# Performance work log

Hardware: AMD Instinct MI355X
Metric: run time of the kernel (lower is better)

## Reference

```python
import jax, jax.numpy as jnp
import numpy as np

B, L = 4096, 200
N_USERS, N_ITEMS, N_CATS, N_DUR = 200000, 500000, 1000, 20
D = 64  # item_embed_dim == seq_embed_dim


def _lin(k, din, dout):
    kw, kb = jax.random.split(k)
    s = 1.0 / np.sqrt(din)
    return (jax.random.uniform(kw, (din, dout), minval=-s, maxval=s),
            jax.random.uniform(kb, (dout,), minval=-s, maxval=s))


def setup_inputs() -> dict:
    key = jax.random.key(0)
    ks = jax.random.split(key, 20)
    inp = {
        'user_id': jax.random.randint(ks[0], (B,), 0, N_USERS),
        'item_id': jax.random.randint(ks[1], (B,), 0, N_ITEMS),
        'item_category': jax.random.randint(ks[2], (B,), 0, N_CATS),
        'item_dur_bkt': jax.random.randint(ks[3], (B,), 0, N_DUR),
        'user_dense': jax.random.normal(ks[4], (B, 25), dtype=jnp.float32),
        'item_dense': jax.random.normal(ks[5], (B, 3), dtype=jnp.float32),
        'history_seq': jax.random.randint(ks[6], (B, L), 0, N_ITEMS + 1),
        # embedding tables (init std=0.01 as in _init_weights)
        'user_W': 0.01 * jax.random.normal(ks[7], (N_USERS, 64), dtype=jnp.float32),
        'item_W': 0.01 * jax.random.normal(ks[8], (N_ITEMS, D), dtype=jnp.float32),
        'cat_W': 0.01 * jax.random.normal(ks[9], (N_CATS, 16), dtype=jnp.float32),
        'dur_W': 0.01 * jax.random.normal(ks[10], (N_DUR, 8), dtype=jnp.float32),
        'hist_W': 0.01 * jax.random.normal(ks[11], (N_ITEMS + 1, D), dtype=jnp.float32),
    }
    # attention MLP: 4*D=256 -> 64 -> 32 -> 1
    inp['aW0'], inp['ab0'] = _lin(ks[12], 4 * D, 64)
    inp['aW1'], inp['ab1'] = _lin(ks[13], 64, 32)
    inp['aW2'], inp['ab2'] = _lin(ks[14], 32, 1)
    # final MLP: concat_dim 64+64+16+8+25+3+64 = 244 -> 256 -> 128 -> 1
    inp['mW0'], inp['mb0'] = _lin(ks[15], 244, 256)
    inp['mW1'], inp['mb1'] = _lin(ks[16], 256, 128)
    inp['mW2'], inp['mb2'] = _lin(ks[17], 128, 1)
    return inp


def reference(user_id, item_id, item_category, item_dur_bkt, user_dense, item_dense,
              history_seq, user_W, item_W, cat_W, dur_W, hist_W,
              aW0, ab0, aW1, ab1, aW2, ab2, mW0, mb0, mW1, mb1, mW2, mb2):
    u_emb = user_W[user_id]            # (B, 64)
    i_emb = item_W[item_id]            # (B, D)
    c_emb = cat_W[item_category]       # (B, 16)
    d_emb = dur_W[item_dur_bkt]        # (B, 8)
    hist = hist_W[history_seq]         # (B, L, D)

    t = i_emb[:, None, :]              # (B, 1, D); item_dim == seq_dim so no slice
    tb = jnp.broadcast_to(t, hist.shape)
    feat = jnp.concatenate([hist, tb, hist * t, hist - t], axis=-1)  # (B, L, 4D)

    h = jax.nn.relu(feat @ aW0 + ab0)
    h = jax.nn.relu(h @ aW1 + ab1)
    scores = (h @ aW2 + ab2)[..., 0]   # (B, L)

    pad_mask = history_seq == 0
    scores = jnp.where(pad_mask, jnp.float32(-1e9), scores)
    w = jax.nn.softmax(scores, axis=-1)                # (B, L)
    pooled = jnp.einsum('bl,bld->bd', w, hist)         # (B, D)

    x = jnp.concatenate([u_emb, i_emb, c_emb, d_emb, user_dense, item_dense, pooled], axis=-1)
    h = jax.nn.relu(x @ mW0 + mb0)     # dropout is identity in eval mode
    h = jax.nn.relu(h @ mW1 + mb1)
    logit = (h @ mW2 + mb2)[..., 0]
    return jax.nn.sigmoid(logit)       # (B,)
```

## Files before the change

kernel.cpp:

```cpp
#include <hip/hip_runtime.h>
#include <hip/hip_bf16.h>

#define L_SZ 200
#define RB 8
#define HS_STRIDE 72

typedef __attribute__((ext_vector_type(8))) short short8;
typedef __attribute__((ext_vector_type(4))) float floatx4;

__device__ __forceinline__ unsigned short f2bf(float f) {
    unsigned int u = __float_as_uint(f);
    unsigned int r = (u + 0x7fffu + ((u >> 16) & 1u)) >> 16;
    return (unsigned short)r;
}
__device__ __forceinline__ float bf2f(unsigned short h) {
    return __uint_as_float(((unsigned int)h) << 16);
}
__device__ __forceinline__ float wave_sum64(float v) {
    #pragma unroll
    for (int m = 1; m <= 32; m <<= 1) v += __shfl_xor(v, m, 64);
    return v;
}
__device__ __forceinline__ float wave_max64(float v) {
    #pragma unroll
    for (int m = 1; m <= 32; m <<= 1) v = fmaxf(v, __shfl_xor(v, m, 64));
    return v;
}
__device__ __forceinline__ unsigned int pk2(float a, float b) {
    return ((unsigned int)f2bf(b) << 16) | (unsigned int)f2bf(a);
}

__global__ __launch_bounds__(256, 4) void attn_kernel(
    const int* __restrict__ item_id, const int* __restrict__ hist_seq,
    const float* __restrict__ item_W, const float* __restrict__ hist_W,
    const float* __restrict__ aW0, const float* __restrict__ ab0,
    const float* __restrict__ aW1, const float* __restrict__ ab1,
    const float* __restrict__ aW2, const float* __restrict__ ab2,
    float* __restrict__ pooled_ws)
{
    __shared__ __align__(16) unsigned char smem[39136];
    unsigned short* Hs  = (unsigned short*)(smem);
    unsigned short* BB  = (unsigned short*)(smem + 28800);
    int*   seq_sh = (int*)(smem + 36992);
    float* scores = (float*)(smem + 37792);
    float* iemb   = (float*)(smem + 38592);
    float* cb     = (float*)(smem + 38848);
    float* red    = (float*)(smem + 39104);

    const int tid  = threadIdx.x;
    const int w    = tid >> 6;
    const int lane = tid & 63;
    const int b    = blockIdx.x;
    const int* hseq = hist_seq + b * L_SZ;

    if (tid < 64)   iemb[tid]   = item_W[(size_t)item_id[b] * 64 + tid];
    if (tid < L_SZ) seq_sh[tid] = hseq[tid];
    __syncthreads();

    for (int u = tid; u < L_SZ * 8; u += 256) {
        int row = u >> 3, c8 = u & 7;
        const float* src = hist_W + (size_t)seq_sh[row] * 64 + c8 * 8;
        float4 f0 = *(const float4*)src;
        float4 f1 = *(const float4*)(src + 4);
        uint4 pk;
        pk.x = pk2(f0.x, f0.y); pk.y = pk2(f0.z, f0.w);
        pk.z = pk2(f1.x, f1.y); pk.w = pk2(f1.z, f1.w);
        *(uint4*)(Hs + row * HS_STRIDE + c8 * 8) = pk;
    }
    for (int u = tid; u < 512; u += 256) {
        int j = u >> 3, k8 = u & 7;
        float v[8];
        #pragma unroll
        for (int i = 0; i < 8; ++i) {
            int k = k8 * 8 + i;
            v[i] = aW0[k * 64 + j] + aW0[(192 + k) * 64 + j]
                 + iemb[k] * aW0[(128 + k) * 64 + j];
        }
        uint4 pk;
        pk.x = pk2(v[0], v[1]); pk.y = pk2(v[2], v[3]);
        pk.z = pk2(v[4], v[5]); pk.w = pk2(v[6], v[7]);
        *(uint4*)(BB + j * 64 + (k8 ^ (j & 7)) * 8) = pk;
    }
    if (w < 2) {
        float cpart = 0.f;
        #pragma unroll 4
        for (int t = 0; t < 32; ++t) {
            int k = w * 32 + t;
            cpart = fmaf(iemb[k], aW0[(64 + k) * 64 + lane] - aW0[(192 + k) * 64 + lane], cpart);
        }
        scores[w * 64 + lane] = cpart;
    }
    const int c = lane & 15, q = lane >> 4;
    short8 bW1[2][2];
    #pragma unroll
    for (int nt = 0; nt < 2; ++nt)
        #pragma unroll
        for (int ks = 0; ks < 2; ++ks) {
            unsigned short tmp[8];
            #pragma unroll
            for (int i = 0; i < 8; ++i)
                tmp[i] = f2bf(aW1[(ks * 32 + q * 8 + i) * 32 + nt * 16 + c]);
            bW1[nt][ks] = *(short8*)tmp;
        }
    float ab1r[2], aw2r[2];
    #pragma unroll
    for (int nt = 0; nt < 2; ++nt) {
        ab1r[nt] = ab1[nt * 16 + c];
        aw2r[nt] = aW2[nt * 16 + c];
    }
    const float ab2s = ab2[0];
    __syncthreads();

    short8 bW[4][2];
    #pragma unroll
    for (int nt = 0; nt < 4; ++nt)
        #pragma unroll
        for (int ks = 0; ks < 2; ++ks)
            bW[nt][ks] = *(const short8*)(BB + (nt * 16 + c) * 64
                                             + ((4 * ks + q) ^ (c & 7)) * 8);
    if (tid < 64)
        cb[tid] = ab0[tid] + scores[tid] + scores[64 + tid];
    __syncthreads();

    float cbr[4];
    #pragma unroll
    for (int nt = 0; nt < 4; ++nt) cbr[nt] = cb[nt * 16 + c];
    unsigned short* scrw = BB + w * (16 * 64);
    const floatx4 zf = {0.f, 0.f, 0.f, 0.f};

    for (int mt = w; mt < 13; mt += 4) {
        const int rowbase = mt * 16;
        floatx4 acc0[4] = {zf, zf, zf, zf};
        #pragma unroll
        for (int ks = 0; ks < 2; ++ks) {
            short8 a = *(const short8*)(Hs + (rowbase + c) * HS_STRIDE + ks * 32 + q * 8);
            acc0[0] = __builtin_amdgcn_mfma_f32_16x16x32_bf16(a, bW[0][ks], acc0[0], 0, 0, 0);
            acc0[1] = __builtin_amdgcn_mfma_f32_16x16x32_bf16(a, bW[1][ks], acc0[1], 0, 0, 0);
            acc0[2] = __builtin_amdgcn_mfma_f32_16x16x32_bf16(a, bW[2][ks], acc0[2], 0, 0, 0);
            acc0[3] = __builtin_amdgcn_mfma_f32_16x16x32_bf16(a, bW[3][ks], acc0[3], 0, 0, 0);
        }
        #pragma unroll
        for (int nt = 0; nt < 4; ++nt)
            #pragma unroll
            for (int r = 0; r < 4; ++r) {
                float h = fmaxf(acc0[nt][r] + cbr[nt], 0.f);
                int row = q * 4 + r;
                int gp = (2 * nt + (c >> 3)) ^ (row & 7);
                scrw[row * 64 + gp * 8 + (c & 7)] = f2bf(h);
            }
        floatx4 acc1[2] = {zf, zf};
        #pragma unroll
        for (int ks = 0; ks < 2; ++ks) {
            short8 a1 = *(const short8*)(scrw + c * 64 + ((4 * ks + q) ^ (c & 7)) * 8);
            acc1[0] = __builtin_amdgcn_mfma_f32_16x16x32_bf16(a1, bW1[0][ks], acc1[0], 0, 0, 0);
            acc1[1] = __builtin_amdgcn_mfma_f32_16x16x32_bf16(a1, bW1[1][ks], acc1[1], 0, 0, 0);
        }
        float s[4];
        #pragma unroll
        for (int r = 0; r < 4; ++r)
            s[r] = fmaxf(acc1[0][r] + ab1r[0], 0.f) * aw2r[0]
                 + fmaxf(acc1[1][r] + ab1r[1], 0.f) * aw2r[1];
        #pragma unroll
        for (int m = 1; m <= 8; m <<= 1)
            #pragma unroll
            for (int r = 0; r < 4; ++r) s[r] += __shfl_xor(s[r], m, 64);
        if (c == 0) {
            #pragma unroll
            for (int r = 0; r < 4; ++r) {
                int l = rowbase + q * 4 + r;
                if (l < L_SZ)
                    scores[l] = (seq_sh[l] == 0) ? -1.0e9f : (s[r] + ab2s);
            }
        }
    }
    __syncthreads();

    float s0 = (tid < L_SZ) ? scores[tid] : -3.0e38f;
    float mx = wave_max64(s0);
    if (lane == 0) red[w] = mx;
    __syncthreads();
    mx = fmaxf(fmaxf(red[0], red[1]), fmaxf(red[2], red[3]));
    float e = (tid < L_SZ) ? __expf(s0 - mx) : 0.f;
    float sm = wave_sum64(e);
    if (lane == 0) red[4 + w] = sm;
    __syncthreads();
    const float winv = 1.f / ((red[4] + red[5]) + (red[6] + red[7]));
    if (tid < L_SZ) scores[tid] = e * winv;
    __syncthreads();

    float* pools = (float*)BB;
    {
        int g  = (w << 1) | (lane >> 5);
        int jj = lane & 31;
        int l0 = g * 26, l1 = (l0 + 26 < L_SZ) ? l0 + 26 : L_SZ;
        float p0 = 0.f, p1 = 0.f;
        for (int l = l0; l < l1; ++l) {
            float wt = scores[l];
            unsigned int pv = *(const unsigned int*)(Hs + l * HS_STRIDE + jj * 2);
            p0 = fmaf(wt, bf2f((unsigned short)(pv & 0xffffu)), p0);
            p1 = fmaf(wt, bf2f((unsigned short)(pv >> 16)), p1);
        }
        float2 pp = {p0, p1};
        *(float2*)&pools[g * 64 + jj * 2] = pp;
    }
    __syncthreads();
    if (tid < 64) {
        float sum = 0.f;
        #pragma unroll
        for (int g = 0; g < 8; ++g) sum += pools[g * 64 + tid];
        pooled_ws[(size_t)b * 64 + tid] = sum;
    }
}

__global__ __launch_bounds__(256) void mlp_kernel(
    const int* __restrict__ user_id, const int* __restrict__ item_id,
    const int* __restrict__ item_cat, const int* __restrict__ item_dur,
    const float* __restrict__ user_dense, const float* __restrict__ item_dense,
    const float* __restrict__ user_W, const float* __restrict__ item_W,
    const float* __restrict__ cat_W, const float* __restrict__ dur_W,
    const float* __restrict__ mW0, const float* __restrict__ mb0,
    const float* __restrict__ mW1, const float* __restrict__ mb1,
    const float* __restrict__ mW2, const float* __restrict__ mb2,
    const float* __restrict__ pooled_ws, float* __restrict__ out)
{
    __shared__ __align__(16) float xT[244][RB];
    __shared__ __align__(16) float h0T[256][RB];
    __shared__ __align__(16) float h1T[128][RB];
    __shared__ __align__(16) float part[128][RB];

    const int tid = threadIdx.x;
    const int b0 = blockIdx.x * RB;

    for (int idx = tid; idx < 244 * RB; idx += 256) {
        int r = idx / 244;
        int c = idx - r * 244;
        int b = b0 + r;
        float v;
        if (c < 64)       v = user_W[(size_t)user_id[b] * 64 + c];
        else if (c < 128) v = item_W[(size_t)item_id[b] * 64 + (c - 64)];
        else if (c < 144) v = cat_W[item_cat[b] * 16 + (c - 128)];
        else if (c < 152) v = dur_W[item_dur[b] * 8 + (c - 144)];
        else if (c < 177) v = user_dense[b * 25 + (c - 152)];
        else if (c < 180) v = item_dense[b * 3 + (c - 177)];
        else              v = pooled_ws[(size_t)b * 64 + (c - 180)];
        xT[c][r] = v;
    }
    __syncthreads();

    {
        float acc[RB];
        const float bias = mb0[tid];
        #pragma unroll
        for (int r = 0; r < RB; ++r) acc[r] = bias;
        #pragma unroll 4
        for (int k = 0; k < 244; ++k) {
            float wk = mW0[k * 256 + tid];
            float4 xa = *(const float4*)&xT[k][0];
            float4 xb = *(const float4*)&xT[k][4];
            acc[0] = fmaf(wk, xa.x, acc[0]);
            acc[1] = fmaf(wk, xa.y, acc[1]);
            acc[2] = fmaf(wk, xa.z, acc[2]);
            acc[3] = fmaf(wk, xa.w, acc[3]);
            acc[4] = fmaf(wk, xb.x, acc[4]);
            acc[5] = fmaf(wk, xb.y, acc[5]);
            acc[6] = fmaf(wk, xb.z, acc[6]);
            acc[7] = fmaf(wk, xb.w, acc[7]);
        }
        #pragma unroll
        for (int r = 0; r < RB; ++r) h0T[tid][r] = fmaxf(acc[r], 0.f);
    }
    __syncthreads();

    const int jj = tid & 127;
    const int half = tid >> 7;
    {
        float acc[RB];
        #pragma unroll
        for (int r = 0; r < RB; ++r) acc[r] = 0.f;
        #pragma unroll 4
        for (int t = 0; t < 128; ++t) {
            int k = half * 128 + t;
            float wk = mW1[k * 128 + jj];
            float4 ha = *(const float4*)&h0T[k][0];
            float4 hb = *(const float4*)&h0T[k][4];
            acc[0] = fmaf(wk, ha.x, acc[0]);
            acc[1] = fmaf(wk, ha.y, acc[1]);
            acc[2] = fmaf(wk, ha.z, acc[2]);
            acc[3] = fmaf(wk, ha.w, acc[3]);
            acc[4] = fmaf(wk, hb.x, acc[4]);
            acc[5] = fmaf(wk, hb.y, acc[5]);
            acc[6] = fmaf(wk, hb.z, acc[6]);
            acc[7] = fmaf(wk, hb.w, acc[7]);
        }
        if (half == 1) {
            #pragma unroll
            for (int r = 0; r < RB; ++r) part[jj][r] = acc[r];
        }
        __syncthreads();
        if (half == 0) {
            const float bias = mb1[jj];
            #pragma unroll
            for (int r = 0; r < RB; ++r)
                h1T[jj][r] = fmaxf(acc[r] + part[jj][r] + bias, 0.f);
        }
    }
    __syncthreads();

    if (tid < RB) {
        const int r = tid;
        float a0 = mb2[0], a1 = 0.f;
        #pragma unroll 8
        for (int k = 0; k < 128; k += 2) {
            a0 = fmaf(h1T[k][r],     mW2[k],     a0);
            a1 = fmaf(h1T[k + 1][r], mW2[k + 1], a1);
        }
        float a = a0 + a1;
        out[b0 + r] = 1.f / (1.f + __expf(-a));
    }
}

extern "C" void kernel_launch(void* const* d_in, const int* in_sizes, int n_in,
                              void* d_out, int out_size, void* d_ws, size_t ws_size,
                              hipStream_t stream) {
    (void)in_sizes; (void)n_in; (void)out_size; (void)ws_size;
    const int*   user_id    = (const int*)d_in[0];
    const int*   item_id    = (const int*)d_in[1];
    const int*   item_cat   = (const int*)d_in[2];
    const int*   item_dur   = (const int*)d_in[3];
    const float* user_dense = (const float*)d_in[4];
    const float* item_dense = (const float*)d_in[5];
    const int*   hist_seq   = (const int*)d_in[6];
    const float* user_W     = (const float*)d_in[7];
    const float* item_W     = (const float*)d_in[8];
    const float* cat_W      = (const float*)d_in[9];
    const float* dur_W      = (const float*)d_in[10];
    const float* hist_W     = (const float*)d_in[11];
    const float* aW0 = (const float*)d_in[12];
    const float* ab0 = (const float*)d_in[13];
    const float* aW1 = (const float*)d_in[14];
    const float* ab1 = (const float*)d_in[15];
    const float* aW2 = (const float*)d_in[16];
    const float* ab2 = (const float*)d_in[17];
    const float* mW0 = (const float*)d_in[18];
    const float* mb0 = (const float*)d_in[19];
    const float* mW1 = (const float*)d_in[20];
    const float* mb1 = (const float*)d_in[21];
    const float* mW2 = (const float*)d_in[22];
    const float* mb2 = (const float*)d_in[23];
    float* out = (float*)d_out;
    float* pooled_ws = (float*)d_ws;

    attn_kernel<<<4096, 256, 0, stream>>>(item_id, hist_seq, item_W, hist_W,
                                          aW0, ab0, aW1, ab1, aW2, ab2, pooled_ws);
    mlp_kernel<<<4096 / RB, 256, 0, stream>>>(user_id, item_id, item_cat, item_dur,
                                              user_dense, item_dense,
                                              user_W, item_W, cat_W, dur_W,
                                              mW0, mb0, mW1, mb1, mW2, mb2,
                                              pooled_ws, out);
}
```

Before: 431.2 us.

## Gather history rows directly into MFMA A-fragments and drop sync stages

Each wave now gathers its own history rows from global memory straight into registers shaped as MFMA A operands. It packs them to bf16 and uses them directly for the first attention layer, storing a swizzled copy to shared memory only for the pooling step. The shared item-embedding and sequence buffers, one barrier and the serial gather-then-convert phase are removed, and the hist loads are issued early to overlap with the weight preparation. The cost is higher register pressure from holding up to four tiles of gathered floats per thread, which may reduce occupancy.

```diff
diff --git a/kernel.cpp b/kernel.cpp
--- a/kernel.cpp
+++ b/kernel.cpp
@@ -3,7 +3,6 @@
 
 #define L_SZ 200
 #define RB 8
-#define HS_STRIDE 72
 
 typedef __attribute__((ext_vector_type(8))) short short8;
 typedef __attribute__((ext_vector_type(4))) float floatx4;
@@ -38,43 +37,71 @@
     const float* __restrict__ aW2, const float* __restrict__ ab2,
     float* __restrict__ pooled_ws)
 {
-    __shared__ __align__(16) unsigned char smem[39136];
-    unsigned short* Hs  = (unsigned short*)(smem);
-    unsigned short* BB  = (unsigned short*)(smem + 28800);
-    int*   seq_sh = (int*)(smem + 36992);
-    float* scores = (float*)(smem + 37792);
-    float* iemb   = (float*)(smem + 38592);
-    float* cb     = (float*)(smem + 38848);
-    float* red    = (float*)(smem + 39104);
+    __shared__ __align__(16) unsigned char smem[35136];
+    unsigned short* Hs = (unsigned short*)(smem);
+    unsigned short* BB = (unsigned short*)(smem + 25600);
+    float* scores = (float*)(smem + 33792);
+    float* cbp    = (float*)(smem + 34592);
+    float* red    = (float*)(smem + 35104);
 
     const int tid  = threadIdx.x;
     const int w    = tid >> 6;
     const int lane = tid & 63;
+    const int c    = lane & 15, q = lane >> 4;
     const int b    = blockIdx.x;
-    const int* hseq = hist_seq + b * L_SZ;
-
-    if (tid < 64)   iemb[tid]   = item_W[(size_t)item_id[b] * 64 + tid];
-    if (tid < L_SZ) seq_sh[tid] = hseq[tid];
-    __syncthreads();
-
-    for (int u = tid; u < L_SZ * 8; u += 256) {
-        int row = u >> 3, c8 = u & 7;
-        const float* src = hist_W + (size_t)seq_sh[row] * 64 + c8 * 8;
-        float4 f0 = *(const float4*)src;
-        float4 f1 = *(const float4*)(src + 4);
-        uint4 pk;
-        pk.x = pk2(f0.x, f0.y); pk.y = pk2(f0.z, f0.w);
-        pk.z = pk2(f1.x, f1.y); pk.w = pk2(f1.z, f1.w);
-        *(uint4*)(Hs + row * HS_STRIDE + c8 * 8) = pk;
-    }
+    const int item = item_id[b];
+    const float* iW = item_W + (size_t)item * 64;
+
+    const int ntile = (w == 0) ? 4 : 3;
+
+    int    seqr[4];
+    float4 g0[4][2], g1[4][2];
+    #pragma unroll
+    for (int t = 0; t < 4; ++t) {
+        if (t < ntile) {
+            const int mt  = w + 4 * t;
+            const int row = mt * 16 + c;
+            const int rc  = (row < L_SZ) ? row : (L_SZ - 1);
+            seqr[t] = hist_seq[b * L_SZ + rc];
+            const float* hrow = hist_W + (size_t)seqr[t] * 64;
+            #pragma unroll
+            for (int ks = 0; ks < 2; ++ks) {
+                g0[t][ks] = *(const float4*)(hrow + ks * 32 + q * 8);
+                g1[t][ks] = *(const float4*)(hrow + ks * 32 + q * 8 + 4);
+            }
+        }
+    }
+
+    short8 bW1[2][2];
+    #pragma unroll
+    for (int nt = 0; nt < 2; ++nt)
+        #pragma unroll
+        for (int ks = 0; ks < 2; ++ks) {
+            unsigned short tmp[8];
+            #pragma unroll
+            for (int i = 0; i < 8; ++i)
+                tmp[i] = f2bf(aW1[(ks * 32 + q * 8 + i) * 32 + nt * 16 + c]);
+            bW1[nt][ks] = *(short8*)tmp;
+        }
+    float ab1r[2], aw2r[2];
+    #pragma unroll
+    for (int nt = 0; nt < 2; ++nt) {
+        ab1r[nt] = ab1[nt * 16 + c];
+        aw2r[nt] = aW2[nt * 16 + c];
+    }
+    const float ab2s = ab2[0];
+
     for (int u = tid; u < 512; u += 256) {
         int j = u >> 3, k8 = u & 7;
+        float4 ia = *(const float4*)(iW + k8 * 8);
+        float4 ib = *(const float4*)(iW + k8 * 8 + 4);
+        float ie[8] = {ia.x, ia.y, ia.z, ia.w, ib.x, ib.y, ib.z, ib.w};
         float v[8];
         #pragma unroll
         for (int i = 0; i < 8; ++i) {
             int k = k8 * 8 + i;
             v[i] = aW0[k * 64 + j] + aW0[(192 + k) * 64 + j]
-                 + iemb[k] * aW0[(128 + k) * 64 + j];
+                 + ie[i] * aW0[(128 + k) * 64 + j];
         }
         uint4 pk;
         pk.x = pk2(v[0], v[1]); pk.y = pk2(v[2], v[3]);
@@ -86,29 +113,30 @@
         #pragma unroll 4
         for (int t = 0; t < 32; ++t) {
             int k = w * 32 + t;
-            cpart = fmaf(iemb[k], aW0[(64 + k) * 64 + lane] - aW0[(192 + k) * 64 + lane], cpart);
-        }
-        scores[w * 64 + lane] = cpart;
-    }
-    const int c = lane & 15, q = lane >> 4;
-    short8 bW1[2][2];
-    #pragma unroll
-    for (int nt = 0; nt < 2; ++nt)
-        #pragma unroll
-        for (int ks = 0; ks < 2; ++ks) {
-            unsigned short tmp[8];
-            #pragma unroll
-            for (int i = 0; i < 8; ++i)
-                tmp[i] = f2bf(aW1[(ks * 32 + q * 8 + i) * 32 + nt * 16 + c]);
-            bW1[nt][ks] = *(short8*)tmp;
-        }
-    float ab1r[2], aw2r[2];
-    #pragma unroll
-    for (int nt = 0; nt < 2; ++nt) {
-        ab1r[nt] = ab1[nt * 16 + c];
-        aw2r[nt] = aW2[nt * 16 + c];
-    }
-    const float ab2s = ab2[0];
+            cpart = fmaf(iW[k], aW0[(64 + k) * 64 + lane] - aW0[(192 + k) * 64 + lane], cpart);
+        }
+        cbp[w * 64 + lane] = cpart;
+    }
+
+    short8 afr[4][2];
+    #pragma unroll
+    for (int t = 0; t < 4; ++t) {
+        if (t < ntile) {
+            const int mt  = w + 4 * t;
+            const int row = mt * 16 + c;
+            #pragma unroll
+            for (int ks = 0; ks < 2; ++ks) {
+                uint4 pk;
+                pk.x = pk2(g0[t][ks].x, g0[t][ks].y);
+                pk.y = pk2(g0[t][ks].z, g0[t][ks].w);
+                pk.z = pk2(g1[t][ks].x, g1[t][ks].y);
+                pk.w = pk2(g1[t][ks].z, g1[t][ks].w);
+                afr[t][ks] = *(short8*)&pk;
+                if (row < L_SZ)
+                    *(uint4*)(Hs + row * 64 + ((ks * 4 + q) ^ (row & 7)) * 8) = pk;
+            }
+        }
+    }
     __syncthreads();
 
     short8 bW[4][2];
@@ -118,26 +146,29 @@
         for (int ks = 0; ks < 2; ++ks)
             bW[nt][ks] = *(const short8*)(BB + (nt * 16 + c) * 64
                                              + ((4 * ks + q) ^ (c & 7)) * 8);
-    if (tid < 64)
-        cb[tid] = ab0[tid] + scores[tid] + scores[64 + tid];
-    __syncthreads();
-
     float cbr[4];
     #pragma unroll
-    for (int nt = 0; nt < 4; ++nt) cbr[nt] = cb[nt * 16 + c];
+    for (int nt = 0; nt < 4; ++nt) {
+        int j = nt * 16 + c;
+        cbr[nt] = ab0[j] + cbp[j] + cbp[64 + j];
+    }
+    __syncthreads();
+
     unsigned short* scrw = BB + w * (16 * 64);
     const floatx4 zf = {0.f, 0.f, 0.f, 0.f};
 
-    for (int mt = w; mt < 13; mt += 4) {
+    #pragma unroll
+    for (int t = 0; t < 4; ++t) {
+        if (t >= ntile) break;
+        const int mt = w + 4 * t;
         const int rowbase = mt * 16;
         floatx4 acc0[4] = {zf, zf, zf, zf};
         #pragma unroll
         for (int ks = 0; ks < 2; ++ks) {
-            short8 a = *(const short8*)(Hs + (rowbase + c) * HS_STRIDE + ks * 32 + q * 8);
-            acc0[0] = __builtin_amdgcn_mfma_f32_16x16x32_bf16(a, bW[0][ks], acc0[0], 0, 0, 0);
-            acc0[1] = __builtin_amdgcn_mfma_f32_16x16x32_bf16(a, bW[1][ks], acc0[1], 0, 0, 0);
-            acc0[2] = __builtin_amdgcn_mfma_f32_16x16x32_bf16(a, bW[2][ks], acc0[2], 0, 0, 0);
-            acc0[3] = __builtin_amdgcn_mfma_f32_16x16x32_bf16(a, bW[3][ks], acc0[3], 0, 0, 0);
+            acc0[0] = __builtin_amdgcn_mfma_f32_16x16x32_bf16(afr[t][ks], bW[0][ks], acc0[0], 0, 0, 0);
+            acc0[1] = __builtin_amdgcn_mfma_f32_16x16x32_bf16(afr[t][ks], bW[1][ks], acc0[1], 0, 0, 0);
+            acc0[2] = __builtin_amdgcn_mfma_f32_16x16x32_bf16(afr[t][ks], bW[2][ks], acc0[2], 0, 0, 0);
+            acc0[3] = __builtin_amdgcn_mfma_f32_16x16x32_bf16(afr[t][ks], bW[3][ks], acc0[3], 0, 0, 0);
         }
         #pragma unroll
         for (int nt = 0; nt < 4; ++nt)
@@ -164,13 +195,13 @@
         for (int m = 1; m <= 8; m <<= 1)
             #pragma unroll
             for (int r = 0; r < 4; ++r) s[r] += __shfl_xor(s[r], m, 64);
-        if (c == 0) {
-            #pragma unroll
-            for (int r = 0; r < 4; ++r) {
-                int l = rowbase + q * 4 + r;
-                if (l < L_SZ)
-                    scores[l] = (seq_sh[l] == 0) ? -1.0e9f : (s[r] + ab2s);
-            }
+        int rsel = c & 3;
+        float sv = (rsel == 0) ? s[0] : (rsel == 1) ? s[1] : (rsel == 2) ? s[2] : s[3];
+        sv = __shfl(sv, ((c >> 2) << 4) | c, 64);
+        if (q == 0) {
+            int l = rowbase + c;
+            if (l < L_SZ)
+                scores[l] = (seqr[t] == 0) ? -1.0e9f : (sv + ab2s);
         }
     }
     __syncthreads();
@@ -196,7 +227,8 @@
         float p0 = 0.f, p1 = 0.f;
         for (int l = l0; l < l1; ++l) {
             float wt = scores[l];
-            unsigned int pv = *(const unsigned int*)(Hs + l * HS_STRIDE + jj * 2);
+            int grp = (jj >> 2) ^ (l & 7);
+            unsigned int pv = *(const unsigned int*)(Hs + l * 64 + grp * 8 + ((2 * jj) & 7));
             p0 = fmaf(wt, bf2f((unsigned short)(pv & 0xffffu)), p0);
             p1 = fmaf(wt, bf2f((unsigned short)(pv >> 16)), p1);
         }
```

Result: slower. 485.8 us (+12.7%).
